# Performance work log

Hardware: AMD Instinct MI355X
Metric: run time of the kernel (lower is better)

Reference implementation:

```python
import jax, jax.numpy as jnp
import numpy as np

A, NA, D_OBS, B = 16, 8, 64, 128  # agents, actions, obs dim, graphs
DZ = D_OBS + NA  # obs_z_input_dim = 72


def _mlp(x, W1, b1, W2, b2):
    # Linear -> leaky_relu(0.01) -> Linear, torch Linear convention (y = x @ W.T + b)
    return jax.nn.leaky_relu(x @ W1.T + b1) @ W2.T + b2


def setup_inputs() -> dict:
    key = jax.random.key(0)
    ks = iter(jax.random.split(key, 40))
    p = {}
    p["obs"] = jax.random.normal(next(ks), (B * A, D_OBS), jnp.float32)
    p["policies"] = jax.random.uniform(next(ks), (B * A, NA), jnp.float32)
    p["actions"] = jax.random.uniform(next(ks), (B * A, NA), jnp.float32)

    def mk(name, inp, out):
        p[name + "_w"] = jax.random.normal(next(ks), (out, inp), jnp.float32) / np.sqrt(inp).astype(np.float32)
        p[name + "_b"] = jax.random.normal(next(ks), (out,), jnp.float32) * 0.01

    mk("kw1", D_OBS, 64); mk("kw2", 64, 64)   # key_weight layers
    mk("qw1", D_OBS, 64); mk("qw2", 64, 64)   # query_weight layers
    mk("ko1", DZ, 64);    mk("ko2", 64, 64)   # key_obsz layers
    mk("qo1", DZ, 64);    mk("qo2", 64, 64)   # query_obsz layers
    mk("av1", DZ, 64);    mk("av2", 64, 64)   # attention_value_obsz layers
    mk("fv1", 128, 64);   mk("fv2", 64, 8)    # final_value layers
    return p


def reference(obs, policies, actions,
              kw1_w, kw1_b, kw2_w, kw2_b, qw1_w, qw1_b, qw2_w, qw2_b,
              ko1_w, ko1_b, ko2_w, ko2_b, qo1_w, qo1_b, qo2_w, qo2_b,
              av1_w, av1_b, av2_w, av2_b, fv1_w, fv1_b, fv2_w, fv2_b):
    d_k_w = jnp.sqrt(jnp.float32(kw2_w.shape[0]))
    d_k_o = jnp.sqrt(jnp.float32(ko2_w.shape[0]))
    Bn = obs.shape[0] // A
    obs_b = obs.reshape(Bn, A, -1)                      # [B,A,Dobs]
    pi = policies.reshape(Bn, A, NA)
    act = actions.reshape(Bn, A, NA)

    # --- DGL update_all on the fully-connected (with self-loop) per-batch graph ---
    key_z = _mlp(obs_b, kw1_w, kw1_b, kw2_w, kw2_b)     # [B,A,dk]
    query_z = _mlp(obs_b, qw1_w, qw1_b, qw2_w, qw2_b)
    score = jnp.einsum('bjd,bid->bij', key_z, query_z)  # src key j -> dst query i
    w = jax.nn.sigmoid(score / d_k_w)[..., None]        # [B,A,A,1], mailbox gate
    z = w * act[:, None] + (1.0 - w) * pi[:, None]      # [B,A(i),A(j),NA]
    weight_z = w.reshape(Bn * A, A, 1)

    # obs_z[b,i,j] = cat(obs[b,j], z[b,i,j])
    obs_rep = jnp.broadcast_to(obs_b[:, None], (Bn, A, A, obs_b.shape[-1]))
    obs_z = jnp.concatenate([obs_rep, z], axis=-1)      # [B,A,A,DZ]

    diag = jnp.arange(A)
    src = obs_z[:, diag, diag]                          # source_obs_z_: [B,A,DZ] (j==i entry)

    key_o = _mlp(src, ko1_w, ko1_b, ko2_w, ko2_b)       # broadcast over j
    query_o = _mlp(obs_z, qo1_w, qo1_b, qo2_w, qo2_b)   # [B,A,A,dk]
    score_o = jnp.einsum('bid,bijd->bij', key_o, query_o)
    weights_o = jax.nn.softmax(jnp.exp(jnp.clip(score_o / d_k_o, -5.0, 5.0)), axis=-1)  # [B,A,A]

    # obs_z_pi[b,i,j,k] = op[b,j] if k==j else obs_z[b,i,k], op = cat(obs, pi)
    op = jnp.concatenate([obs_b, pi], axis=-1)          # [B,A,DZ]
    m = jnp.eye(A, dtype=obs.dtype)[None, None, :, :, None]          # (j,k) mask
    obs_z_pi = obs_z[:, :, None] * (1.0 - m) + op[:, None, None] * m  # [B,A,A,A,DZ]

    attn_src = _mlp(src, av1_w, av1_b, av2_w, av2_b)                  # [B,A,O]
    attn_other = _mlp(obs_z_pi, av1_w, av1_b, av2_w, av2_b)           # [B,A,A,A,O]

    w_exp = weights_o[:, None, :, :, None]              # [b,i,j,k,1] = weights_o[b,j,k]
    mixed = jnp.mean(attn_other * w_exp, axis=-2)       # mean over k -> [B,A,A,O]
    src_rep = jnp.broadcast_to(attn_src[:, None], mixed.shape)
    node_features = jnp.concatenate([src_rep, mixed], axis=-1)        # [B,A,A,2O]
    value = _mlp(node_features, fv1_w, fv1_b, fv2_w, fv2_b)           # [B,A,A,8]

    weights_obsz = jnp.broadcast_to(w_exp, (Bn, A, A, A, 1))
    return value, weight_z, weights_obsz
```

## Files before the change

kernel.cpp:

```cpp
#include <hip/hip_runtime.h>

#define A_ 16
#define NA_ 8
#define DOBS_ 64

typedef _Float16 f16;
typedef f16 h2 __attribute__((ext_vector_type(2)));
typedef f16 v8h __attribute__((ext_vector_type(8)));
typedef float v4f __attribute__((ext_vector_type(4)));

__device__ __forceinline__ float fdot2f(h2 a, h2 b, float c) {
  return __builtin_amdgcn_fdot2(a, b, c, false);
}
__device__ __forceinline__ float lrelu(float x) { return x > 0.f ? x : 0.01f * x; }

struct P {
  const float *obs, *pol, *act;
  const float *kw1w, *kw1b, *kw2w, *kw2b, *qw1w, *qw1b, *qw2w, *qw2b;
  const float *ko1w, *ko1b, *ko2w, *ko2b, *qo1w, *qo1b, *qo2w, *qo2b;
  const float *av1w, *av1b, *av2w, *av2b, *fv1w, *fv1b, *fv2w, *fv2b;
  float *out0, *out1, *out2;
};

#define OBSH 0
#define OBSL 1152
#define X1Ho 2304
#define X1Lo 3456
#define X2Ho 4608
#define X2Lo 5760
#define EHO  6912
#define FLT  7168
#define F_PI   0
#define F_ACT  128
#define F_WSIG 256
#define F_WO   512
#define F_C0   768
#define F_S2   784
#define F_S3G  1872
#define F_WZK  2960
#define F_WZQ  3472
#define F_B    3984
#define WKW1  15648
#define WQW1  20256
#define WKW2  24864
#define WQW2  29472
#define WKO1H 34080
#define WKO1L 38688
#define WKO2H 43296
#define WKO2L 47904
#define WQO1H 52512
#define WQO1L 57120
#define WQO2H 61728
#define WQO2L 66336
#define AV1H  15648
#define AV2H  21792
#define BACKB1 26400
#define SLA   26656
#define SLB   70944
#define AOSRC 77088
#define APTO  78240
#define FV1H  34080
#define FV2PW 42784
#define BACKB2 43296
#define LDS_F16 79776

__device__ __forceinline__ v4f gemm_plain(const f16* Xh, const f16* W, float bv, int nt, int lane) {
  const int m = lane & 15, q = lane >> 4;
  v4f acc = {bv, bv, bv, bv};
  const v8h a0 = *(const v8h*)(Xh + m * 72 + q * 8);
  const v8h a1 = *(const v8h*)(Xh + m * 72 + 32 + q * 8);
  const f16* wr = W + (nt * 16 + m) * 72 + q * 8;
  acc = __builtin_amdgcn_mfma_f32_16x16x32_f16(a0, *(const v8h*)wr, acc, 0, 0, 0);
  acc = __builtin_amdgcn_mfma_f32_16x16x32_f16(a1, *(const v8h*)(wr + 32), acc, 0, 0, 0);
  return acc;
}

__device__ __forceinline__ v4f gemm_tile(const f16* Xh, const f16* Xl,
                                         const f16* Wh, const f16* Wl,
                                         float bv, int nt, int lane) {
  const int m = lane & 15, q = lane >> 4;
  v4f acc = {bv, bv, bv, bv};
  const v8h ah0 = *(const v8h*)(Xh + m * 72 + q * 8);
  const v8h ah1 = *(const v8h*)(Xh + m * 72 + 32 + q * 8);
  const v8h al0 = *(const v8h*)(Xl + m * 72 + q * 8);
  const v8h al1 = *(const v8h*)(Xl + m * 72 + 32 + q * 8);
  const f16* wr = Wh + (nt * 16 + m) * 72 + q * 8;
  const v8h bh0 = *(const v8h*)(wr);
  const v8h bh1 = *(const v8h*)(wr + 32);
  const f16* wr2 = Wl + (nt * 16 + m) * 72 + q * 8;
  const v8h bl0 = *(const v8h*)(wr2);
  const v8h bl1 = *(const v8h*)(wr2 + 32);
  acc = __builtin_amdgcn_mfma_f32_16x16x32_f16(ah0, bh0, acc, 0, 0, 0);
  acc = __builtin_amdgcn_mfma_f32_16x16x32_f16(ah1, bh1, acc, 0, 0, 0);
  acc = __builtin_amdgcn_mfma_f32_16x16x32_f16(ah0, bl0, acc, 0, 0, 0);
  acc = __builtin_amdgcn_mfma_f32_16x16x32_f16(ah1, bl1, acc, 0, 0, 0);
  acc = __builtin_amdgcn_mfma_f32_16x16x32_f16(al0, bh0, acc, 0, 0, 0);
  acc = __builtin_amdgcn_mfma_f32_16x16x32_f16(al1, bh1, acc, 0, 0, 0);
  return acc;
}

__device__ __forceinline__ void writeX(f16* Xh, f16* Xl, v4f acc, int nt, int lane, bool relu) {
  const int m = lane & 15, q = lane >> 4;
#pragma unroll
  for (int reg = 0; reg < 4; reg++) {
    float y = acc[reg];
    if (relu) y = lrelu(y);
    const f16 yh = (f16)y;
    Xh[(q * 4 + reg) * 72 + nt * 16 + m] = yh;
    Xl[(q * 4 + reg) * 72 + nt * 16 + m] = (f16)(y - (float)yh);
  }
}

__device__ __forceinline__ void putP(f16* W, float4 v, int o, int rq) {
  h2* d = (h2*)(W + o * 72 + 4 * rq);
  d[0] = h2{(f16)v.x, (f16)v.y};
  d[1] = h2{(f16)v.z, (f16)v.w};
}

__device__ __forceinline__ void putW(f16* Wh, f16* Wl, float4 v, int o, int rq) {
  h2* dh = (h2*)(Wh + o * 72 + 4 * rq);
  h2* dl = (h2*)(Wl + o * 72 + 4 * rq);
  const f16 hx = (f16)v.x, hy = (f16)v.y, hz = (f16)v.z, hw = (f16)v.w;
  dh[0] = h2{hx, hy};
  dh[1] = h2{hz, hw};
  dl[0] = h2{(f16)(v.x - (float)hx), (f16)(v.y - (float)hy)};
  dl[1] = h2{(f16)(v.z - (float)hz), (f16)(v.w - (float)hw)};
}

__device__ __forceinline__ v8h bfrag(const f16* Wm, int stride, int nt, int ks, int lane) {
  const int n = lane & 15, q = lane >> 4;
  return *(const v8h*)(Wm + (nt * 16 + n) * stride + ks * 32 + q * 8);
}

__device__ __forceinline__ void av_mlp2(const f16* obsh, const f16* av1H, const f16* av2H,
                                        const float* av1b, const float* av2b,
                                        f16* Hbuf, v8h az, int lane, v4f acc2[4]) {
  const int m = lane & 15, q = lane >> 4;
  const v8h a0 = *(const v8h*)(obsh + m * 72 + q * 8);
  const v8h a1 = *(const v8h*)(obsh + m * 72 + 32 + q * 8);
#pragma unroll
  for (int nt = 0; nt < 4; nt++) {
    const float bv = av1b[nt * 16 + m];
    v4f acc = {bv, bv, bv, bv};
    acc = __builtin_amdgcn_mfma_f32_16x16x32_f16(a0, bfrag(av1H, 96, nt, 0, lane), acc, 0, 0, 0);
    acc = __builtin_amdgcn_mfma_f32_16x16x32_f16(a1, bfrag(av1H, 96, nt, 1, lane), acc, 0, 0, 0);
    acc = __builtin_amdgcn_mfma_f32_16x16x32_f16(az, bfrag(av1H, 96, nt, 2, lane), acc, 0, 0, 0);
#pragma unroll
    for (int reg = 0; reg < 4; reg++)
      Hbuf[(q * 4 + reg) * 72 + nt * 16 + m] = (f16)lrelu(acc[reg]);
  }
  const v8h h0 = *(const v8h*)(Hbuf + m * 72 + q * 8);
  const v8h h1 = *(const v8h*)(Hbuf + m * 72 + 32 + q * 8);
#pragma unroll
  for (int nt = 0; nt < 4; nt++) {
    const float bv = av2b[nt * 16 + m];
    v4f acc = {bv, bv, bv, bv};
    acc = __builtin_amdgcn_mfma_f32_16x16x32_f16(h0, bfrag(av2H, 72, nt, 0, lane), acc, 0, 0, 0);
    acc = __builtin_amdgcn_mfma_f32_16x16x32_f16(h1, bfrag(av2H, 72, nt, 1, lane), acc, 0, 0, 0);
    acc2[nt] = acc;
  }
}

__global__ __launch_bounds__(512) void critic_fused(P p) {
  extern __shared__ f16 SMB[];
  float* F = (float*)(SMB + FLT);
  const int tid = threadIdx.x;
  const int b = blockIdx.x >> 1, ihalf = blockIdx.x & 1;
  const int w = tid >> 6, lane = tid & 63;
  const int m = lane & 15, quad = lane >> 4;
  const int o = tid & 63, r8 = tid >> 6;

  const float2 Robs = ((const float2*)(p.obs + (size_t)b * 1024))[tid];
  float Rpa = 0.f;
  if (tid < 128) Rpa = p.pol[(size_t)b * 128 + tid];
  else if (tid < 256) Rpa = p.act[(size_t)b * 128 + tid - 128];
  const float Rwzko = p.ko1w[(tid >> 3) * 72 + 64 + (tid & 7)];
  const float Rwzqo = p.qo1w[(tid >> 3) * 72 + 64 + (tid & 7)];
  float4 Rkw1[2], Rqw1[2], Rkw2[2], Rqw2[2], Rko1[2], Rko2[2], Rqo1[2], Rqo2[2];
#pragma unroll
  for (int h = 0; h < 2; h++) {
    const int rq = r8 + 8 * h;
    Rkw1[h] = *(const float4*)(p.kw1w + o * 64 + 4 * rq);
    Rqw1[h] = *(const float4*)(p.qw1w + o * 64 + 4 * rq);
    Rkw2[h] = *(const float4*)(p.kw2w + o * 64 + 4 * rq);
    Rqw2[h] = *(const float4*)(p.qw2w + o * 64 + 4 * rq);
    Rko1[h] = *(const float4*)(p.ko1w + o * 72 + 4 * rq);
    Rko2[h] = *(const float4*)(p.ko2w + o * 64 + 4 * rq);
    Rqo1[h] = *(const float4*)(p.qo1w + o * 72 + 4 * rq);
    Rqo2[h].x = p.qo2w[(4 * rq + 0) * 64 + o];
    Rqo2[h].y = p.qo2w[(4 * rq + 1) * 64 + o];
    Rqo2[h].z = p.qo2w[(4 * rq + 2) * 64 + o];
    Rqo2[h].w = p.qo2w[(4 * rq + 3) * 64 + o];
  }
  const int bi = (w & 3) * 16 + m;
  const float bias1 = (w < 4 ? p.kw1b : p.qw1b)[bi];
  const float bias2 = (w < 4 ? p.kw2b : p.qw2b)[bi];
  float rbo1 = 0.f, rbo2 = 0.f, rbo3 = 0.f, rbo4 = 0.f;
  if (tid < 64) { rbo1 = p.ko1b[tid]; rbo2 = p.ko2b[tid]; rbo3 = p.qo1b[tid]; rbo4 = p.qo2b[tid]; }
  const float4 rav1a = ((const float4*)p.av1w)[tid * 2];
  const float4 rav1b = ((const float4*)p.av1w)[tid * 2 + 1];
  const float rav1c = p.av1w[4096 + tid];
  const float4 rav2a = ((const float4*)p.av2w)[tid * 2];
  const float4 rav2b = ((const float4*)p.av2w)[tid * 2 + 1];
  float4 rfv[4];
#pragma unroll
  for (int qq = 0; qq < 4; qq++) rfv[qq] = ((const float4*)p.fv1w)[tid * 4 + qq];
  const float rfv2 = p.fv2w[tid];
  float rb1 = 0.f, rb2 = 0.f, rb3 = 0.f, rb4 = 0.f;
  if (tid < 64) { rb1 = p.av1b[tid]; rb2 = p.av2b[tid]; rb3 = p.fv1b[tid]; }
  if (tid < 8) rb4 = p.fv2b[tid];

  {
    const int e0 = 2 * tid, r0 = e0 >> 6, c0i = e0 & 63;
    const f16 hx = (f16)Robs.x, hy = (f16)Robs.y;
    *(h2*)(SMB + OBSH + r0 * 72 + c0i) = h2{hx, hy};
    *(h2*)(SMB + OBSL + r0 * 72 + c0i) = h2{(f16)(Robs.x - (float)hx), (f16)(Robs.y - (float)hy)};
  }
  if (tid < 128) F[F_PI + tid] = Rpa;
  else if (tid < 256) F[F_ACT + tid - 128] = Rpa;
  F[F_WZK + tid] = Rwzko;
  { const int oo = tid >> 3, c = tid & 7; F[F_WZQ + (oo & 15) * 32 + (oo >> 4) * 8 + c] = Rwzqo; }
  if (tid < 64) {
    F[F_B + tid] = rbo1; F[F_B + 64 + tid] = rbo2;
    F[F_B + 128 + tid] = rbo3; F[F_B + 192 + tid] = rbo4;
  }
#pragma unroll
  for (int h = 0; h < 2; h++) {
    const int rq = r8 + 8 * h;
    putP(SMB + WKW1, Rkw1[h], o, rq);
    putP(SMB + WQW1, Rqw1[h], o, rq);
    putP(SMB + WKW2, Rkw2[h], o, rq);
    putP(SMB + WQW2, Rqw2[h], o, rq);
    putW(SMB + WKO1H, SMB + WKO1L, Rko1[h], o, rq);
    putW(SMB + WKO2H, SMB + WKO2L, Rko2[h], o, rq);
    putW(SMB + WQO1H, SMB + WQO1L, Rqo1[h], o, rq);
    putW(SMB + WQO2H, SMB + WQO2L, Rqo2[h], o, rq);
  }
  __syncthreads();

  {
    const f16* Wp = (w < 4) ? (SMB + WKW1) : (SMB + WQW1);
    f16* Xo = (w < 4) ? (SMB + X1Ho) : (SMB + X2Ho);
    v4f a = gemm_plain(SMB + OBSH, Wp, bias1, w & 3, lane);
#pragma unroll
    for (int reg = 0; reg < 4; reg++)
      Xo[(quad * 4 + reg) * 72 + (w & 3) * 16 + m] = (f16)lrelu(a[reg]);
  }
  __syncthreads();

  {
    const f16* Wp = (w < 4) ? (SMB + WKW2) : (SMB + WQW2);
    const f16* Xi = (w < 4) ? (SMB + X1Ho) : (SMB + X2Ho);
    float* So = (w < 4) ? (F + F_S2) : (F + F_S3G);
    v4f a = gemm_plain(Xi, Wp, bias2, w & 3, lane);
#pragma unroll
    for (int reg = 0; reg < 4; reg++)
      So[(quad * 4 + reg) * 68 + (w & 3) * 16 + m] = a[reg];
  }
  __syncthreads();

  {
    const int idx = tid >> 1, g2 = tid & 1;
    const int i = idx >> 4, j = idx & 15;
    float a0 = 0.f, a1 = 0.f, a2 = 0.f, a3 = 0.f;
#pragma unroll
    for (int t4 = 0; t4 < 8; t4++) {
      const float4 qv = *(const float4*)(F + F_S3G + i * 68 + g2 * 32 + 4 * t4);
      const float4 kv = *(const float4*)(F + F_S2 + j * 68 + g2 * 32 + 4 * t4);
      a0 += qv.x * kv.x; a1 += qv.y * kv.y; a2 += qv.z * kv.z; a3 += qv.w * kv.w;
    }
    float sc = (a0 + a1) + (a2 + a3);
    sc += __shfl_xor(sc, 1);
    if (g2 == 0) {
      const float wv = 1.f / (1.f + __expf(-sc * 0.125f));
      F[F_WSIG + idx] = wv;
      p.out1[(size_t)b * 256 + idx] = wv;
    }
  }
  {
    float av1v[8] = {rav1a.x, rav1a.y, rav1a.z, rav1a.w, rav1b.x, rav1b.y, rav1b.z, rav1b.w};
#pragma unroll
    for (int e = 0; e < 8; e++) {
      const int k = tid * 8 + e, rr = k / 72, cc = k - rr * 72;
      SMB[AV1H + rr * 96 + cc] = (f16)av1v[e];
    }
    const int k = 4096 + tid, rr = k / 72, cc = k - rr * 72;
    SMB[AV1H + rr * 96 + cc] = (f16)rav1c;
    const int row = tid >> 3, c0p = 72 + (tid & 7) * 3;
#pragma unroll
    for (int c = 0; c < 3; c++) SMB[AV1H + row * 96 + c0p + c] = (f16)0.f;
    float av2v[8] = {rav2a.x, rav2a.y, rav2a.z, rav2a.w, rav2b.x, rav2b.y, rav2b.z, rav2b.w};
#pragma unroll
    for (int e = 0; e < 8; e++) {
      const int k2 = tid * 8 + e;
      SMB[AV2H + (k2 >> 6) * 72 + (k2 & 63)] = (f16)av2v[e];
    }
    float* BF1w = (float*)(SMB + BACKB1);
    if (tid < 64) { BF1w[tid] = rb1; BF1w[64 + tid] = rb2; }
  }
  __syncthreads();

  const float* BF1 = (const float*)(SMB + BACKB1);
  auto do_av_task = [&](int t) {
    f16* Hb;
    v8h az = {};
    if (t < 8) {
      Hb = (t < 4) ? (SMB + SLA + t * 1536) : (SMB + SLB + (t - 4) * 1536);
      if (quad == 0) {
        const float wv = F[F_WSIG + (ihalf * 8 + t) * 16 + m];
#pragma unroll
        for (int c = 0; c < 8; c++)
          az[c] = (f16)(F[F_PI + m * 8 + c] + wv * (F[F_ACT + m * 8 + c] - F[F_PI + m * 8 + c]));
      }
    } else if (t == 8) {
      Hb = SMB + APTO;
      if (quad == 0) {
#pragma unroll
        for (int c = 0; c < 8; c++) az[c] = (f16)F[F_PI + m * 8 + c];
      }
    } else {
      Hb = SMB + AOSRC;
      if (quad == 0) {
        const float wv = F[F_WSIG + m * 17];
#pragma unroll
        for (int c = 0; c < 8; c++)
          az[c] = (f16)(F[F_PI + m * 8 + c] + wv * (F[F_ACT + m * 8 + c] - F[F_PI + m * 8 + c]));
      }
    }
    v4f acc2[4];
    av_mlp2(SMB + OBSH, SMB + AV1H, SMB + AV2H, BF1, BF1 + 64, Hb, az, lane, acc2);
    if (t < 9) {
#pragma unroll
      for (int nt = 0; nt < 4; nt++)
#pragma unroll
        for (int reg = 0; reg < 4; reg++)
          Hb[(nt * 16 + m) * 24 + quad * 4 + reg] = (f16)acc2[nt][reg];
    } else {
#pragma unroll
      for (int nt = 0; nt < 4; nt++)
#pragma unroll
        for (int reg = 0; reg < 4; reg++)
          SMB[AOSRC + (quad * 4 + reg) * 72 + nt * 16 + m] = (f16)acc2[nt][reg];
    }
  };

  if (w < 2) {
#pragma unroll
    for (int k2 = 0; k2 < 2; k2++) {
      const int nt = w * 2 + k2;
      v4f a = gemm_tile(SMB + OBSH, SMB + OBSL, SMB + WKO1H, SMB + WKO1L, F[F_B + nt * 16 + m], nt, lane);
      const int oo = nt * 16 + m;
      float wzv[8];
      *(float4*)wzv = *(const float4*)(F + F_WZK + oo * 8);
      *(float4*)(wzv + 4) = *(const float4*)(F + F_WZK + oo * 8 + 4);
#pragma unroll
      for (int reg = 0; reg < 4; reg++) {
        const int rr = quad * 4 + reg;
        const float wrr = F[F_WSIG + rr * 17];
        float zp = 0.f;
#pragma unroll
        for (int c = 0; c < 8; c++) {
          const float zc = F[F_PI + rr * 8 + c] + wrr * (F[F_ACT + rr * 8 + c] - F[F_PI + rr * 8 + c]);
          zp += wzv[c] * zc;
        }
        const float y = lrelu(a[reg] + zp);
        const f16 yh = (f16)y;
        SMB[X2Ho + rr * 72 + oo] = yh;
        SMB[X2Lo + rr * 72 + oo] = (f16)(y - (float)yh);
      }
    }
  } else if (w < 4) {
#pragma unroll
    for (int k2 = 0; k2 < 2; k2++) {
      const int nt = (w - 2) * 2 + k2;
      v4f a = gemm_tile(SMB + OBSH, SMB + OBSL, SMB + WQO1H, SMB + WQO1L, F[F_B + 128 + nt * 16 + m], nt, lane);
#pragma unroll
      for (int reg = 0; reg < 4; reg++)
        F[F_S3G + m * 68 + (quad * 4 + reg) * 4 + nt] = a[reg];
    }
  } else {
    do_av_task(w - 4);
  }
  __syncthreads();

  if (w < 2) {
#pragma unroll
    for (int k2 = 0; k2 < 2; k2++) {
      const int nt = w * 2 + k2;
      v4f a = gemm_tile(SMB + X2Ho, SMB + X2Lo, SMB + WKO2H, SMB + WKO2L, F[F_B + 64 + nt * 16 + m], nt, lane);
      writeX(SMB + X1Ho, SMB + X1Lo, a, nt, lane, false);
    }
  } else if (w == 2) {
    do_av_task(8);
  } else if (w == 3) {
    do_av_task(9);
  } else {
    do_av_task(w);
  }
  __syncthreads();

  if (w < 2) {
#pragma unroll
    for (int k2 = 0; k2 < 2; k2++) {
      const int nt = w * 2 + k2;
      v4f a = gemm_tile(SMB + X1Ho, SMB + X1Lo, SMB + WQO2H, SMB + WQO2L, 0.f, nt, lane);
#pragma unroll
      for (int reg = 0; reg < 4; reg++)
        F[F_S2 + (quad * 4 + reg) * 68 + nt * 16 + m] = a[reg];
    }
    {
      const int rr = tid >> 3, cs = (tid & 7) * 8;
      float t = 0.f;
#pragma unroll
      for (int c = 0; c < 8; c++) {
        const float kv = (float)SMB[X1Ho + rr * 72 + cs + c] + (float)SMB[X1Lo + rr * 72 + cs + c];
        t += kv * F[F_B + 192 + cs + c];
      }
      t += __shfl_xor(t, 1);
      t += __shfl_xor(t, 2);
      t += __shfl_xor(t, 4);
      if ((tid & 7) == 0) F[F_C0 + rr] = t;
    }
  }
  __syncthreads();

  {
    const int idx = tid >> 1, g2 = tid & 1;
    const int i = idx >> 4, j = idx & 15;
    const float wij = F[F_WSIG + i * 16 + j];
    float z[8];
#pragma unroll
    for (int c = 0; c < 8; c++)
      z[c] = F[F_PI + j * 8 + c] + wij * (F[F_ACT + j * 8 + c] - F[F_PI + j * 8 + c]);
    float sc = 0.f;
#pragma unroll
    for (int gg = 2 * g2; gg <= 2 * g2 + 1; gg++) {
#pragma unroll
      for (int t = 0; t < 16; t++) {
        const float4 wa = *(const float4*)(F + F_WZQ + t * 32 + gg * 8);
        const float4 wb = *(const float4*)(F + F_WZQ + t * 32 + gg * 8 + 4);
        float hv = F[F_S3G + t * 68 + j * 4 + gg]
          + wa.x * z[0] + wa.y * z[1] + wa.z * z[2] + wa.w * z[3]
          + wb.x * z[4] + wb.y * z[5] + wb.z * z[6] + wb.w * z[7];
        hv = lrelu(hv);
        sc += F[F_S2 + i * 68 + gg * 16 + t] * hv;
      }
    }
    sc += __shfl_xor(sc, 1);
    if (g2 == 0) {
      float yv = (sc + F[F_C0 + i]) * 0.125f;
      yv = fminf(fmaxf(yv, -5.f), 5.f);
      SMB[EHO + idx] = (f16)__expf(yv);
    }
  }
  __syncthreads();

  if (tid < 256) {
    const int i = tid >> 4, j = tid & 15;
    float ev[16]; float mx = -1e30f;
#pragma unroll
    for (int jj = 0; jj < 16; jj++) { ev[jj] = (float)SMB[EHO + i * 16 + jj]; mx = fmaxf(mx, ev[jj]); }
    float den = 0.f;
#pragma unroll
    for (int jj = 0; jj < 16; jj++) den += __expf(ev[jj] - mx);
    F[F_WO + tid] = __expf(ev[j] - mx) / den;
  }
#pragma unroll
  for (int qq = 0; qq < 4; qq++) {
    const int e0 = tid * 16 + qq * 4;
    h2* d = (h2*)&SMB[FV1H + (e0 >> 7) * 136 + (e0 & 127)];
    d[0] = h2{(f16)rfv[qq].x, (f16)rfv[qq].y};
    d[1] = h2{(f16)rfv[qq].z, (f16)rfv[qq].w};
  }
  SMB[FV2PW + tid] = (f16)rfv2;
  {
    float* BF2w = (float*)(SMB + BACKB2);
    if (tid < 64) BF2w[tid] = rb3;
    if (tid < 8) BF2w[64 + tid] = rb4;
  }
  __syncthreads();

  {
    const float* BF2 = (const float*)(SMB + BACKB2);
    const int i_ = ihalf * 8 + w;
    f16* Sl = (w < 4) ? (SMB + SLA + w * 1536) : (SMB + SLB + (w - 4) * 1536);
    v8h am;
#pragma unroll
    for (int e = 0; e < 8; e++) {
      const int j2 = quad * 8 + e;
      float v;
      if (j2 < 16) v = F[F_WO + m * 16 + j2] * 0.0625f;
      else v = (j2 - 16 == m) ? F[F_WO + m * 17] * 0.0625f : 0.f;
      am[e] = (f16)v;
    }
    {
      v4f macc[4];
#pragma unroll
      for (int nt = 0; nt < 4; nt++) {
        const int oo = nt * 16 + m;
        v8h bf;
        if (quad < 2) {
          bf = *(const v8h*)(Sl + oo * 24 + quad * 8);
        } else {
          const v8h apv = *(const v8h*)(&SMB[APTO + oo * 24 + (quad - 2) * 8]);
          const v8h aov = *(const v8h*)(Sl + oo * 24 + (quad - 2) * 8);
          bf = apv - aov;
        }
        v4f z4 = {0.f, 0.f, 0.f, 0.f};
        macc[nt] = __builtin_amdgcn_mfma_f32_16x16x32_f16(am, bf, z4, 0, 0, 0);
      }
#pragma unroll
      for (int nt = 0; nt < 4; nt++)
#pragma unroll
        for (int reg = 0; reg < 4; reg++)
          Sl[(quad * 4 + reg) * 72 + nt * 16 + m] = (f16)macc[nt][reg];
    }
    {
      const v8h f0 = *(const v8h*)(&SMB[AOSRC + m * 72 + quad * 8]);
      const v8h f1 = *(const v8h*)(&SMB[AOSRC + m * 72 + 32 + quad * 8]);
      const v8h f2 = *(const v8h*)(Sl + m * 72 + quad * 8);
      const v8h f3 = *(const v8h*)(Sl + m * 72 + 32 + quad * 8);
#pragma unroll
      for (int nt = 0; nt < 4; nt++) {
        const float bv = BF2[nt * 16 + m];
        v4f acc = {bv, bv, bv, bv};
        acc = __builtin_amdgcn_mfma_f32_16x16x32_f16(f0, bfrag(SMB + FV1H, 136, nt, 0, lane), acc, 0, 0, 0);
        acc = __builtin_amdgcn_mfma_f32_16x16x32_f16(f1, bfrag(SMB + FV1H, 136, nt, 1, lane), acc, 0, 0, 0);
        acc = __builtin_amdgcn_mfma_f32_16x16x32_f16(f2, bfrag(SMB + FV1H, 136, nt, 2, lane), acc, 0, 0, 0);
        acc = __builtin_amdgcn_mfma_f32_16x16x32_f16(f3, bfrag(SMB + FV1H, 136, nt, 3, lane), acc, 0, 0, 0);
#pragma unroll
        for (int reg = 0; reg < 4; reg++)
          Sl[(quad * 4 + reg) * 72 + nt * 16 + m] = (f16)lrelu(acc[reg]);
      }
    }
    {
      const int g2 = quad;
      float y0 = BF2[64 + 2 * g2], y1 = BF2[64 + 2 * g2 + 1];
#pragma unroll
      for (int o2 = 0; o2 < 32; o2++) {
        const h2 hh = *(const h2*)(Sl + m * 72 + 2 * o2);
        const h2 w0v = *(const h2*)(&SMB[FV2PW + (2 * g2) * 64 + 2 * o2]);
        const h2 w1v = *(const h2*)(&SMB[FV2PW + (2 * g2 + 1) * 64 + 2 * o2]);
        y0 = fdot2f(w0v, hh, y0);
        y1 = fdot2f(w1v, hh, y1);
      }
      *(float2*)(p.out0 + ((size_t)b * 256 + i_ * 16 + m) * 8 + 2 * g2) = make_float2(y0, y1);
    }
    {
      const float4 wv4 = *(const float4*)(F + F_WO + m * 16 + quad * 4);
      *(float4*)(p.out2 + ((size_t)b * 256 + i_ * 16 + m) * 16 + quad * 4) = wv4;
    }
  }
}

extern "C" void kernel_launch(void* const* d_in, const int* in_sizes, int n_in,
                              void* d_out, int out_size, void* d_ws, size_t ws_size,
                              hipStream_t stream) {
  P p;
  p.obs = (const float*)d_in[0];
  p.pol = (const float*)d_in[1];
  p.act = (const float*)d_in[2];
  p.kw1w = (const float*)d_in[3];  p.kw1b = (const float*)d_in[4];
  p.kw2w = (const float*)d_in[5];  p.kw2b = (const float*)d_in[6];
  p.qw1w = (const float*)d_in[7];  p.qw1b = (const float*)d_in[8];
  p.qw2w = (const float*)d_in[9];  p.qw2b = (const float*)d_in[10];
  p.ko1w = (const float*)d_in[11]; p.ko1b = (const float*)d_in[12];
  p.ko2w = (const float*)d_in[13]; p.ko2b = (const float*)d_in[14];
  p.qo1w = (const float*)d_in[15]; p.qo1b = (const float*)d_in[16];
  p.qo2w = (const float*)d_in[17]; p.qo2b = (const float*)d_in[18];
  p.av1w = (const float*)d_in[19]; p.av1b = (const float*)d_in[20];
  p.av2w = (const float*)d_in[21]; p.av2b = (const float*)d_in[22];
  p.fv1w = (const float*)d_in[23]; p.fv1b = (const float*)d_in[24];
  p.fv2w = (const float*)d_in[25]; p.fv2b = (const float*)d_in[26];

  const int Bn = in_sizes[0] / (A_ * DOBS_);
  p.out0 = (float*)d_out;
  p.out1 = p.out0 + (size_t)Bn * A_ * A_ * NA_;
  p.out2 = p.out1 + (size_t)Bn * A_ * A_;

  const size_t lds_bytes = (size_t)LDS_F16 * sizeof(f16);
  (void)hipFuncSetAttribute(reinterpret_cast<const void*>(critic_fused),
                            hipFuncAttributeMaxDynamicSharedMemorySize, (int)lds_bytes);
  hipLaunchKernelGGL(critic_fused, dim3(2 * Bn), dim3(512), lds_bytes, stream, p);
}
```

Baseline: 125.8 us.

## Process each graph in one 1024-thread block instead of two half blocks

Each block now covers a full batch graph with 16 waves, replacing the old split of each graph across two 512-thread blocks that both repeated the shared prologue. The shared setup (weight staging, key/query MLPs, obs-z attention scores) is now done once per graph and spread across twice as many threads, and the 16 attention-value slices are packed into a reorganised LDS layout. The cost is half as many blocks (128 on a device with many CUs), so fewer CUs are busy, and every barrier now waits on 16 waves.

Result: slower. 135.0 us (+7.3%).

```diff
diff --git a/kernel.cpp b/kernel.cpp
--- a/kernel.cpp
+++ b/kernel.cpp
@@ -55,14 +55,23 @@
 #define AV1H  15648
 #define AV2H  21792
 #define BACKB1 26400
-#define SLA   26656
-#define SLB   70944
-#define AOSRC 77088
-#define APTO  78240
-#define FV1H  34080
-#define FV2PW 42784
-#define BACKB2 43296
-#define LDS_F16 79776
+#define SL03  27936
+#define SL47  70944
+#define SL813 34080
+#define SL1415 52512
+#define APTO  55584
+#define AOSRC 57120
+#define FV1H  43296
+#define FV2PW 52000
+#define BACKB2 77088
+#define LDS_F16 77232
+
+__device__ __forceinline__ f16* slice_ptr(f16* SMB, int t) {
+  if (t < 4)  return SMB + SL03 + t * 1536;
+  if (t < 8)  return SMB + SL47 + (t - 4) * 1536;
+  if (t < 14) return SMB + SL813 + (t - 8) * 1536;
+  return SMB + SL1415 + (t - 14) * 1536;
+}
 
 __device__ __forceinline__ v4f gemm_plain(const f16* Xh, const f16* W, float bv, int nt, int lane) {
   const int m = lane & 15, q = lane >> 4;
@@ -161,84 +170,81 @@
   }
 }
 
-__global__ __launch_bounds__(512) void critic_fused(P p) {
+__global__ __launch_bounds__(1024, 1) void critic_fused(P p) {
   extern __shared__ f16 SMB[];
   float* F = (float*)(SMB + FLT);
   const int tid = threadIdx.x;
-  const int b = blockIdx.x >> 1, ihalf = blockIdx.x & 1;
+  const int b = blockIdx.x;
   const int w = tid >> 6, lane = tid & 63;
   const int m = lane & 15, quad = lane >> 4;
-  const int o = tid & 63, r8 = tid >> 6;
-
-  const float2 Robs = ((const float2*)(p.obs + (size_t)b * 1024))[tid];
+  const int o = tid & 63, rq = tid >> 6;
+
+  const float Rob = p.obs[(size_t)b * 1024 + tid];
   float Rpa = 0.f;
   if (tid < 128) Rpa = p.pol[(size_t)b * 128 + tid];
   else if (tid < 256) Rpa = p.act[(size_t)b * 128 + tid - 128];
-  const float Rwzko = p.ko1w[(tid >> 3) * 72 + 64 + (tid & 7)];
-  const float Rwzqo = p.qo1w[(tid >> 3) * 72 + 64 + (tid & 7)];
-  float4 Rkw1[2], Rqw1[2], Rkw2[2], Rqw2[2], Rko1[2], Rko2[2], Rqo1[2], Rqo2[2];
-#pragma unroll
-  for (int h = 0; h < 2; h++) {
-    const int rq = r8 + 8 * h;
-    Rkw1[h] = *(const float4*)(p.kw1w + o * 64 + 4 * rq);
-    Rqw1[h] = *(const float4*)(p.qw1w + o * 64 + 4 * rq);
-    Rkw2[h] = *(const float4*)(p.kw2w + o * 64 + 4 * rq);
-    Rqw2[h] = *(const float4*)(p.qw2w + o * 64 + 4 * rq);
-    Rko1[h] = *(const float4*)(p.ko1w + o * 72 + 4 * rq);
-    Rko2[h] = *(const float4*)(p.ko2w + o * 64 + 4 * rq);
-    Rqo1[h] = *(const float4*)(p.qo1w + o * 72 + 4 * rq);
-    Rqo2[h].x = p.qo2w[(4 * rq + 0) * 64 + o];
-    Rqo2[h].y = p.qo2w[(4 * rq + 1) * 64 + o];
-    Rqo2[h].z = p.qo2w[(4 * rq + 2) * 64 + o];
-    Rqo2[h].w = p.qo2w[(4 * rq + 3) * 64 + o];
-  }
+  float Rwzko = 0.f, Rwzqo = 0.f;
+  if (tid < 512) {
+    Rwzko = p.ko1w[(tid >> 3) * 72 + (tid & 7) + 64];
+    Rwzqo = p.qo1w[(tid >> 3) * 72 + (tid & 7) + 64];
+  }
+  const float4 Rkw1 = *(const float4*)(p.kw1w + o * 64 + 4 * rq);
+  const float4 Rqw1 = *(const float4*)(p.qw1w + o * 64 + 4 * rq);
+  const float4 Rkw2 = *(const float4*)(p.kw2w + o * 64 + 4 * rq);
+  const float4 Rqw2 = *(const float4*)(p.qw2w + o * 64 + 4 * rq);
+  const float4 Rko1 = *(const float4*)(p.ko1w + o * 72 + 4 * rq);
+  const float4 Rko2 = *(const float4*)(p.ko2w + o * 64 + 4 * rq);
+  const float4 Rqo1 = *(const float4*)(p.qo1w + o * 72 + 4 * rq);
+  float4 Rqo2;
+  Rqo2.x = p.qo2w[(4 * rq + 0) * 64 + o];
+  Rqo2.y = p.qo2w[(4 * rq + 1) * 64 + o];
+  Rqo2.z = p.qo2w[(4 * rq + 2) * 64 + o];
+  Rqo2.w = p.qo2w[(4 * rq + 3) * 64 + o];
   const int bi = (w & 3) * 16 + m;
   const float bias1 = (w < 4 ? p.kw1b : p.qw1b)[bi];
   const float bias2 = (w < 4 ? p.kw2b : p.qw2b)[bi];
   float rbo1 = 0.f, rbo2 = 0.f, rbo3 = 0.f, rbo4 = 0.f;
   if (tid < 64) { rbo1 = p.ko1b[tid]; rbo2 = p.ko2b[tid]; rbo3 = p.qo1b[tid]; rbo4 = p.qo2b[tid]; }
-  const float4 rav1a = ((const float4*)p.av1w)[tid * 2];
-  const float4 rav1b = ((const float4*)p.av1w)[tid * 2 + 1];
-  const float rav1c = p.av1w[4096 + tid];
-  const float4 rav2a = ((const float4*)p.av2w)[tid * 2];
-  const float4 rav2b = ((const float4*)p.av2w)[tid * 2 + 1];
-  float4 rfv[4];
-#pragma unroll
-  for (int qq = 0; qq < 4; qq++) rfv[qq] = ((const float4*)p.fv1w)[tid * 4 + qq];
-  const float rfv2 = p.fv2w[tid];
+  const float4 rav1 = ((const float4*)p.av1w)[tid];
+  float2 rav1e = make_float2(0.f, 0.f);
+  if (tid < 256) rav1e = ((const float2*)(p.av1w + 4096))[tid];
+  const float4 rav2 = ((const float4*)p.av2w)[tid];
+  float4 rfv[2];
+  rfv[0] = ((const float4*)p.fv1w)[tid * 2];
+  rfv[1] = ((const float4*)p.fv1w)[tid * 2 + 1];
+  float rfv2 = 0.f;
+  if (tid < 512) rfv2 = p.fv2w[tid];
   float rb1 = 0.f, rb2 = 0.f, rb3 = 0.f, rb4 = 0.f;
   if (tid < 64) { rb1 = p.av1b[tid]; rb2 = p.av2b[tid]; rb3 = p.fv1b[tid]; }
   if (tid < 8) rb4 = p.fv2b[tid];
 
   {
-    const int e0 = 2 * tid, r0 = e0 >> 6, c0i = e0 & 63;
-    const f16 hx = (f16)Robs.x, hy = (f16)Robs.y;
-    *(h2*)(SMB + OBSH + r0 * 72 + c0i) = h2{hx, hy};
-    *(h2*)(SMB + OBSL + r0 * 72 + c0i) = h2{(f16)(Robs.x - (float)hx), (f16)(Robs.y - (float)hy)};
+    const f16 hx = (f16)Rob;
+    SMB[OBSH + rq * 72 + o] = hx;
+    SMB[OBSL + rq * 72 + o] = (f16)(Rob - (float)hx);
   }
   if (tid < 128) F[F_PI + tid] = Rpa;
   else if (tid < 256) F[F_ACT + tid - 128] = Rpa;
-  F[F_WZK + tid] = Rwzko;
-  { const int oo = tid >> 3, c = tid & 7; F[F_WZQ + (oo & 15) * 32 + (oo >> 4) * 8 + c] = Rwzqo; }
+  if (tid < 512) {
+    F[F_WZK + tid] = Rwzko;
+    const int oo = tid >> 3, c = tid & 7;
+    F[F_WZQ + (oo & 15) * 32 + (oo >> 4) * 8 + c] = Rwzqo;
+  }
   if (tid < 64) {
     F[F_B + tid] = rbo1; F[F_B + 64 + tid] = rbo2;
     F[F_B + 128 + tid] = rbo3; F[F_B + 192 + tid] = rbo4;
   }
-#pragma unroll
-  for (int h = 0; h < 2; h++) {
-    const int rq = r8 + 8 * h;
-    putP(SMB + WKW1, Rkw1[h], o, rq);
-    putP(SMB + WQW1, Rqw1[h], o, rq);
-    putP(SMB + WKW2, Rkw2[h], o, rq);
-    putP(SMB + WQW2, Rqw2[h], o, rq);
-    putW(SMB + WKO1H, SMB + WKO1L, Rko1[h], o, rq);
-    putW(SMB + WKO2H, SMB + WKO2L, Rko2[h], o, rq);
-    putW(SMB + WQO1H, SMB + WQO1L, Rqo1[h], o, rq);
-    putW(SMB + WQO2H, SMB + WQO2L, Rqo2[h], o, rq);
-  }
-  __syncthreads();
-
-  {
+  putP(SMB + WKW1, Rkw1, o, rq);
+  putP(SMB + WQW1, Rqw1, o, rq);
+  putP(SMB + WKW2, Rkw2, o, rq);
+  putP(SMB + WQW2, Rqw2, o, rq);
+  putW(SMB + WKO1H, SMB + WKO1L, Rko1, o, rq);
+  putW(SMB + WKO2H, SMB + WKO2L, Rko2, o, rq);
+  putW(SMB + WQO1H, SMB + WQO1L, Rqo1, o, rq);
+  putW(SMB + WQO2H, SMB + WQO2L, Rqo2, o, rq);
+  __syncthreads();
+
+  if (w < 8) {
     const f16* Wp = (w < 4) ? (SMB + WKW1) : (SMB + WQW1);
     f16* Xo = (w < 4) ? (SMB + X1Ho) : (SMB + X2Ho);
     v4f a = gemm_plain(SMB + OBSH, Wp, bias1, w & 3, lane);
@@ -248,7 +254,7 @@
   }
   __syncthreads();
 
-  {
+  if (w < 8) {
     const f16* Wp = (w < 4) ? (SMB + WKW2) : (SMB + WQW2);
     const f16* Xi = (w < 4) ? (SMB + X1Ho) : (SMB + X2Ho);
     float* So = (w < 4) ? (F + F_S2) : (F + F_S3G);
@@ -260,40 +266,52 @@
   __syncthreads();
 
   {
-    const int idx = tid >> 1, g2 = tid & 1;
+    const int idx = tid >> 2, g4 = tid & 3;
     const int i = idx >> 4, j = idx & 15;
     float a0 = 0.f, a1 = 0.f, a2 = 0.f, a3 = 0.f;
 #pragma unroll
-    for (int t4 = 0; t4 < 8; t4++) {
-      const float4 qv = *(const float4*)(F + F_S3G + i * 68 + g2 * 32 + 4 * t4);
-      const float4 kv = *(const float4*)(F + F_S2 + j * 68 + g2 * 32 + 4 * t4);
+    for (int t4 = 0; t4 < 4; t4++) {
+      const float4 qv = *(const float4*)(F + F_S3G + i * 68 + g4 * 16 + 4 * t4);
+      const float4 kv = *(const float4*)(F + F_S2 + j * 68 + g4 * 16 + 4 * t4);
       a0 += qv.x * kv.x; a1 += qv.y * kv.y; a2 += qv.z * kv.z; a3 += qv.w * kv.w;
     }
     float sc = (a0 + a1) + (a2 + a3);
     sc += __shfl_xor(sc, 1);
-    if (g2 == 0) {
+    sc += __shfl_xor(sc, 2);
+    if (g4 == 0) {
       const float wv = 1.f / (1.f + __expf(-sc * 0.125f));
       F[F_WSIG + idx] = wv;
       p.out1[(size_t)b * 256 + idx] = wv;
     }
   }
   {
-    float av1v[8] = {rav1a.x, rav1a.y, rav1a.z, rav1a.w, rav1b.x, rav1b.y, rav1b.z, rav1b.w};
-#pragma unroll
-    for (int e = 0; e < 8; e++) {
-      const int k = tid * 8 + e, rr = k / 72, cc = k - rr * 72;
+    float av1v[4] = {rav1.x, rav1.y, rav1.z, rav1.w};
+#pragma unroll
+    for (int e = 0; e < 4; e++) {
+      const int k = tid * 4 + e, rr = k / 72, cc = k - rr * 72;
       SMB[AV1H + rr * 96 + cc] = (f16)av1v[e];
     }
-    const int k = 4096 + tid, rr = k / 72, cc = k - rr * 72;
-    SMB[AV1H + rr * 96 + cc] = (f16)rav1c;
-    const int row = tid >> 3, c0p = 72 + (tid & 7) * 3;
-#pragma unroll
-    for (int c = 0; c < 3; c++) SMB[AV1H + row * 96 + c0p + c] = (f16)0.f;
-    float av2v[8] = {rav2a.x, rav2a.y, rav2a.z, rav2a.w, rav2b.x, rav2b.y, rav2b.z, rav2b.w};
-#pragma unroll
-    for (int e = 0; e < 8; e++) {
-      const int k2 = tid * 8 + e;
-      SMB[AV2H + (k2 >> 6) * 72 + (k2 & 63)] = (f16)av2v[e];
+    if (tid < 256) {
+      float av1w2[2] = {rav1e.x, rav1e.y};
+#pragma unroll
+      for (int e = 0; e < 2; e++) {
+        const int k = 4096 + 2 * tid + e, rr = k / 72, cc = k - rr * 72;
+        SMB[AV1H + rr * 96 + cc] = (f16)av1w2[e];
+      }
+    }
+#pragma unroll
+    for (int e = 0; e < 2; e++) {
+      const int idx2 = 2 * tid + e;
+      if (idx2 < 1536) {
+        const int rr = idx2 / 24, cc = 72 + (idx2 - rr * 24);
+        SMB[AV1H + rr * 96 + cc] = (f16)0.f;
+      }
+    }
+    float av2v[4] = {rav2.x, rav2.y, rav2.z, rav2.w};
+#pragma unroll
+    for (int e = 0; e < 4; e++) {
+      const int k = tid * 4 + e;
+      SMB[AV2H + (k >> 6) * 72 + (k & 63)] = (f16)av2v[e];
     }
     float* BF1w = (float*)(SMB + BACKB1);
     if (tid < 64) { BF1w[tid] = rb1; BF1w[64 + tid] = rb2; }
@@ -304,15 +322,15 @@
   auto do_av_task = [&](int t) {
     f16* Hb;
     v8h az = {};
-    if (t < 8) {
-      Hb = (t < 4) ? (SMB + SLA + t * 1536) : (SMB + SLB + (t - 4) * 1536);
+    if (t < 16) {
+      Hb = slice_ptr(SMB, t);
       if (quad == 0) {
-        const float wv = F[F_WSIG + (ihalf * 8 + t) * 16 + m];
+        const float wv = F[F_WSIG + t * 16 + m];
 #pragma unroll
         for (int c = 0; c < 8; c++)
           az[c] = (f16)(F[F_PI + m * 8 + c] + wv * (F[F_ACT + m * 8 + c] - F[F_PI + m * 8 + c]));
       }
-    } else if (t == 8) {
+    } else if (t == 16) {
       Hb = SMB + APTO;
       if (quad == 0) {
 #pragma unroll
@@ -329,7 +347,7 @@
     }
     v4f acc2[4];
     av_mlp2(SMB + OBSH, SMB + AV1H, SMB + AV2H, BF1, BF1 + 64, Hb, az, lane, acc2);
-    if (t < 9) {
+    if (t < 17) {
 #pragma unroll
       for (int nt = 0; nt < 4; nt++)
 #pragma unroll
@@ -344,88 +362,76 @@
     }
   };
 
-  if (w < 2) {
-#pragma unroll
-    for (int k2 = 0; k2 < 2; k2++) {
-      const int nt = w * 2 + k2;
-      v4f a = gemm_tile(SMB + OBSH, SMB + OBSL, SMB + WKO1H, SMB + WKO1L, F[F_B + nt * 16 + m], nt, lane);
-      const int oo = nt * 16 + m;
-      float wzv[8];
-      *(float4*)wzv = *(const float4*)(F + F_WZK + oo * 8);
-      *(float4*)(wzv + 4) = *(const float4*)(F + F_WZK + oo * 8 + 4);
-#pragma unroll
-      for (int reg = 0; reg < 4; reg++) {
-        const int rr = quad * 4 + reg;
-        const float wrr = F[F_WSIG + rr * 17];
-        float zp = 0.f;
-#pragma unroll
-        for (int c = 0; c < 8; c++) {
-          const float zc = F[F_PI + rr * 8 + c] + wrr * (F[F_ACT + rr * 8 + c] - F[F_PI + rr * 8 + c]);
-          zp += wzv[c] * zc;
-        }
-        const float y = lrelu(a[reg] + zp);
-        const f16 yh = (f16)y;
-        SMB[X2Ho + rr * 72 + oo] = yh;
-        SMB[X2Lo + rr * 72 + oo] = (f16)(y - (float)yh);
-      }
-    }
-  } else if (w < 4) {
-#pragma unroll
-    for (int k2 = 0; k2 < 2; k2++) {
-      const int nt = (w - 2) * 2 + k2;
-      v4f a = gemm_tile(SMB + OBSH, SMB + OBSL, SMB + WQO1H, SMB + WQO1L, F[F_B + 128 + nt * 16 + m], nt, lane);
-#pragma unroll
-      for (int reg = 0; reg < 4; reg++)
-        F[F_S3G + m * 68 + (quad * 4 + reg) * 4 + nt] = a[reg];
-    }
+  if (w < 4) {
+    const int nt = w;
+    v4f a = gemm_tile(SMB + OBSH, SMB + OBSL, SMB + WKO1H, SMB + WKO1L, F[F_B + nt * 16 + m], nt, lane);
+    const int oo = nt * 16 + m;
+    float wzv[8];
+    *(float4*)wzv = *(const float4*)(F + F_WZK + oo * 8);
+    *(float4*)(wzv + 4) = *(const float4*)(F + F_WZK + oo * 8 + 4);
+#pragma unroll
+    for (int reg = 0; reg < 4; reg++) {
+      const int rr = quad * 4 + reg;
+      const float wrr = F[F_WSIG + rr * 17];
+      float zp = 0.f;
+#pragma unroll
+      for (int c = 0; c < 8; c++) {
+        const float zc = F[F_PI + rr * 8 + c] + wrr * (F[F_ACT + rr * 8 + c] - F[F_PI + rr * 8 + c]);
+        zp += wzv[c] * zc;
+      }
+      const float y = lrelu(a[reg] + zp);
+      const f16 yh = (f16)y;
+      SMB[X2Ho + rr * 72 + oo] = yh;
+      SMB[X2Lo + rr * 72 + oo] = (f16)(y - (float)yh);
+    }
+  } else if (w < 8) {
+    const int nt = w - 4;
+    v4f a = gemm_tile(SMB + OBSH, SMB + OBSL, SMB + WQO1H, SMB + WQO1L, F[F_B + 128 + nt * 16 + m], nt, lane);
+#pragma unroll
+    for (int reg = 0; reg < 4; reg++)
+      F[F_S3G + m * 68 + (quad * 4 + reg) * 4 + nt] = a[reg];
   } else {
-    do_av_task(w - 4);
-  }
-  __syncthreads();
-
-  if (w < 2) {
-#pragma unroll
-    for (int k2 = 0; k2 < 2; k2++) {
-      const int nt = w * 2 + k2;
-      v4f a = gemm_tile(SMB + X2Ho, SMB + X2Lo, SMB + WKO2H, SMB + WKO2L, F[F_B + 64 + nt * 16 + m], nt, lane);
-      writeX(SMB + X1Ho, SMB + X1Lo, a, nt, lane, false);
-    }
-  } else if (w == 2) {
-    do_av_task(8);
-  } else if (w == 3) {
-    do_av_task(9);
-  } else {
-    do_av_task(w);
-  }
-  __syncthreads();
-
-  if (w < 2) {
-#pragma unroll
-    for (int k2 = 0; k2 < 2; k2++) {
-      const int nt = w * 2 + k2;
-      v4f a = gemm_tile(SMB + X1Ho, SMB + X1Lo, SMB + WQO2H, SMB + WQO2L, 0.f, nt, lane);
-#pragma unroll
-      for (int reg = 0; reg < 4; reg++)
-        F[F_S2 + (quad * 4 + reg) * 68 + nt * 16 + m] = a[reg];
-    }
-    {
-      const int rr = tid >> 3, cs = (tid & 7) * 8;
-      float t = 0.f;
-#pragma unroll
-      for (int c = 0; c < 8; c++) {
-        const float kv = (float)SMB[X1Ho + rr * 72 + cs + c] + (float)SMB[X1Lo + rr * 72 + cs + c];
-        t += kv * F[F_B + 192 + cs + c];
-      }
-      t += __shfl_xor(t, 1);
-      t += __shfl_xor(t, 2);
-      t += __shfl_xor(t, 4);
-      if ((tid & 7) == 0) F[F_C0 + rr] = t;
-    }
+    do_av_task(w - 8);
+  }
+  __syncthreads();
+
+  if (w < 4) {
+    const int nt = w;
+    v4f a = gemm_tile(SMB + X2Ho, SMB + X2Lo, SMB + WKO2H, SMB + WKO2L, F[F_B + 64 + nt * 16 + m], nt, lane);
+    writeX(SMB + X1Ho, SMB + X1Lo, a, nt, lane, false);
+  } else if (w < 12) {
+    do_av_task(w + 4);
+  } else if (w == 12) {
+    do_av_task(16);
+  } else if (w == 13) {
+    do_av_task(17);
+  }
+  __syncthreads();
+
+  if (w < 4) {
+    const int nt = w;
+    v4f a = gemm_tile(SMB + X1Ho, SMB + X1Lo, SMB + WQO2H, SMB + WQO2L, 0.f, nt, lane);
+#pragma unroll
+    for (int reg = 0; reg < 4; reg++)
+      F[F_S2 + (quad * 4 + reg) * 68 + nt * 16 + m] = a[reg];
+  }
+  if (tid < 128) {
+    const int rr = tid >> 3, cs = (tid & 7) * 8;
+    float t = 0.f;
+#pragma unroll
+    for (int c = 0; c < 8; c++) {
+      const float kv = (float)SMB[X1Ho + rr * 72 + cs + c] + (float)SMB[X1Lo + rr * 72 + cs + c];
+      t += kv * F[F_B + 192 + cs + c];
+    }
+    t += __shfl_xor(t, 1);
+    t += __shfl_xor(t, 2);
+    t += __shfl_xor(t, 4);
+    if ((tid & 7) == 0) F[F_C0 + rr] = t;
   }
   __syncthreads();
 
   {
-    const int idx = tid >> 1, g2 = tid & 1;
+    const int idx = tid >> 2, g4 = tid & 3;
     const int i = idx >> 4, j = idx & 15;
     const float wij = F[F_WSIG + i * 16 + j];
     float z[8];
@@ -434,20 +440,18 @@
       z[c] = F[F_PI + j * 8 + c] + wij * (F[F_ACT + j * 8 + c] - F[F_PI + j * 8 + c]);
     float sc = 0.f;
 #pragma unroll
-    for (int gg = 2 * g2; gg <= 2 * g2 + 1; gg++) {
-#pragma unroll
-      for (int t = 0; t < 16; t++) {
-        const float4 wa = *(const float4*)(F + F_WZQ + t * 32 + gg * 8);
-        const float4 wb = *(const float4*)(F + F_WZQ + t * 32 + gg * 8 + 4);
-        float hv = F[F_S3G + t * 68 + j * 4 + gg]
-          + wa.x * z[0] + wa.y * z[1] + wa.z * z[2] + wa.w * z[3]
-          + wb.x * z[4] + wb.y * z[5] + wb.z * z[6] + wb.w * z[7];
-        hv = lrelu(hv);
-        sc += F[F_S2 + i * 68 + gg * 16 + t] * hv;
-      }
+    for (int t = 0; t < 16; t++) {
+      const float4 wa = *(const float4*)(F + F_WZQ + t * 32 + g4 * 8);
+      const float4 wb = *(const float4*)(F + F_WZQ + t * 32 + g4 * 8 + 4);
+      float hv = F[F_S3G + t * 68 + j * 4 + g4]
+        + wa.x * z[0] + wa.y * z[1] + wa.z * z[2] + wa.w * z[3]
+        + wb.x * z[4] + wb.y * z[5] + wb.z * z[6] + wb.w * z[7];
+      hv = lrelu(hv);
+      sc += F[F_S2 + i * 68 + g4 * 16 + t] * hv;
     }
     sc += __shfl_xor(sc, 1);
-    if (g2 == 0) {
+    sc += __shfl_xor(sc, 2);
+    if (g4 == 0) {
       float yv = (sc + F[F_C0 + i]) * 0.125f;
       yv = fminf(fmaxf(yv, -5.f), 5.f);
       SMB[EHO + idx] = (f16)__expf(yv);
@@ -466,13 +470,13 @@
     F[F_WO + tid] = __expf(ev[j] - mx) / den;
   }
 #pragma unroll
-  for (int qq = 0; qq < 4; qq++) {
-    const int e0 = tid * 16 + qq * 4;
+  for (int qq = 0; qq < 2; qq++) {
+    const int e0 = tid * 8 + qq * 4;
     h2* d = (h2*)&SMB[FV1H + (e0 >> 7) * 136 + (e0 & 127)];
     d[0] = h2{(f16)rfv[qq].x, (f16)rfv[qq].y};
     d[1] = h2{(f16)rfv[qq].z, (f16)rfv[qq].w};
   }
-  SMB[FV2PW + tid] = (f16)rfv2;
+  if (tid < 512) SMB[FV2PW + tid] = (f16)rfv2;
   {
     float* BF2w = (float*)(SMB + BACKB2);
     if (tid < 64) BF2w[tid] = rb3;
@@ -482,8 +486,8 @@
 
   {
     const float* BF2 = (const float*)(SMB + BACKB2);
-    const int i_ = ihalf * 8 + w;
-    f16* Sl = (w < 4) ? (SMB + SLA + w * 1536) : (SMB + SLB + (w - 4) * 1536);
+    const int i_ = w;
+    f16* Sl = slice_ptr(SMB, w);
     v8h am;
 #pragma unroll
     for (int e = 0; e < 8; e++) {
@@ -581,5 +585,5 @@
   const size_t lds_bytes = (size_t)LDS_F16 * sizeof(f16);
   (void)hipFuncSetAttribute(reinterpret_cast<const void*>(critic_fused),
                             hipFuncAttributeMaxDynamicSharedMemorySize, (int)lds_bytes);
-  hipLaunchKernelGGL(critic_fused, dim3(2 * Bn), dim3(512), lds_bytes, stream, p);
-}
+  hipLaunchKernelGGL(critic_fused, dim3(Bn), dim3(1024), lds_bytes, stream, p);
+}
```
